# Performance work log

Hardware: AMD Instinct MI355X
Metric: run time of the kernel (lower is better)

## Reference

```python
import jax, jax.numpy as jnp
import numpy as np

N_NODES = 50000
N_EDGES = 640000
RAW = 128
HID = 256
COORD = 3


def setup_inputs() -> dict:
    key = jax.random.key(0)
    ks = jax.random.split(key, 20)

    def w(k, fan_in, fan_out):
        return (jax.random.normal(k, (fan_in, fan_out), jnp.float32)
                / np.float32(np.sqrt(fan_in)))

    return {
        "edge_index": jax.random.randint(ks[0], (2, N_EDGES), 0, N_NODES, jnp.int64)
        if jax.config.jax_enable_x64 else
        jax.random.randint(ks[0], (2, N_EDGES), 0, N_NODES, jnp.int32),
        "str_feature": jax.random.normal(ks[1], (N_NODES, RAW), jnp.float32),
        "coord_feature": jax.random.normal(ks[2], (N_NODES, COORD), jnp.float32),
        # msg_mlp: Linear(2*RAW+1 -> HID), SiLU, Linear(HID -> HID), SiLU
        "msg_w1": w(ks[3], 2 * RAW + 1, HID), "msg_b1": jnp.zeros((HID,), jnp.float32),
        "msg_w2": w(ks[4], HID, HID), "msg_b2": jnp.zeros((HID,), jnp.float32),
        # trans_mlp: Linear(HID->HID), SiLU, Linear(HID->HID), SiLU, Linear(HID->1, no bias, xavier gain=0.001)
        "tr_w1": w(ks[5], HID, HID), "tr_b1": jnp.zeros((HID,), jnp.float32),
        "tr_w2": w(ks[6], HID, HID), "tr_b2": jnp.zeros((HID,), jnp.float32),
        "tr_w3": w(ks[7], HID, 1) * np.float32(0.001),
        # posi_mlp: Linear(RAW+HID->HID), SiLU, Linear(HID->RAW)
        "posi_w1": w(ks[8], RAW + HID, HID), "posi_b1": jnp.zeros((HID,), jnp.float32),
        "posi_w2": w(ks[9], HID, RAW), "posi_b2": jnp.zeros((RAW,), jnp.float32),
    }


def reference(edge_index, str_feature, coord_feature,
              msg_w1, msg_b1, msg_w2, msg_b2,
              tr_w1, tr_b1, tr_w2, tr_b2, tr_w3,
              posi_w1, posi_b1, posi_w2, posi_b2):
    silu = jax.nn.silu
    row, col = edge_index[0], edge_index[1]
    n = str_feature.shape[0]

    # coord2dist
    coord_diff = coord_feature[row] - coord_feature[col]          # [E, 3]
    sqr_dist = jnp.sum(coord_diff * coord_diff, axis=1, keepdims=True)  # [E, 1]

    # msg_model
    edge_in = jnp.concatenate([str_feature[row], str_feature[col], sqr_dist], axis=1)
    msg = silu(silu(edge_in @ msg_w1 + msg_b1) @ msg_w2 + msg_b2)  # [E, HID]

    # coord_model: trans = coord_diff * trans_mlp(msg); x += segment_mean(trans, row)
    gate = silu(silu(msg @ tr_w1 + tr_b1) @ tr_w2 + tr_b2) @ tr_w3  # [E, 1]
    trans = coord_diff * gate                                       # [E, 3]
    trans_sum = jax.ops.segment_sum(trans, row, num_segments=n)     # [N, 3]
    cnt = jax.ops.segment_sum(jnp.ones((trans.shape[0],), trans.dtype), row,
                              num_segments=n)
    trans_mean = trans_sum / jnp.clip(cnt, 1.0)[:, None]
    coord_out = coord_feature + trans_mean

    # posi_model: p + posi_mlp([p, segment_sum(msg, row)])
    msg_sum = jax.ops.segment_sum(msg, row, num_segments=n)         # [N, HID]
    p_in = jnp.concatenate([str_feature, msg_sum], axis=1)
    str_out = str_feature + (silu(p_in @ posi_w1 + posi_b1) @ posi_w2 + posi_b2)

    return str_out, coord_out
```

## Files before the change

### kernel.cpp

```cpp
#include <hip/hip_runtime.h>

#define NN 50000
#define NE 640000

typedef __bf16 bf16x8 __attribute__((ext_vector_type(8)));
typedef short  short8 __attribute__((ext_vector_type(8)));
typedef float  f32x16 __attribute__((ext_vector_type(16)));
typedef float  f32x2  __attribute__((ext_vector_type(2)));
typedef float  f32x4  __attribute__((ext_vector_type(4)));

__device__ __forceinline__ short f2bf(float v) {
  unsigned u = __builtin_bit_cast(unsigned, v);
  u = (u + 0x7FFFu + ((u >> 16) & 1u)) >> 16;
  return (short)u;
}
__device__ __forceinline__ short f2bf_hw(float v) {
  return __builtin_bit_cast(short, (__bf16)v);
}
__device__ __forceinline__ float silu_f(float v) {
  float e = __builtin_amdgcn_exp2f(v * -1.44269504f);
  return v * __builtin_amdgcn_rcpf(1.0f + e);
}
__device__ __forceinline__ bf16x8 ld8(const short* p) {
  return *(const bf16x8*)(p);
}
__device__ __forceinline__ void atomic_add_f(float* p, float v) {
  __hip_atomic_fetch_add(p, v, __ATOMIC_RELAXED, __HIP_MEMORY_SCOPE_AGENT);
}

__global__ void egcl_prep(const float* __restrict__ mw1, const float* __restrict__ mb1,
                          const float* __restrict__ mw2, const float* __restrict__ mb2,
                          const float* __restrict__ tw1, const float* __restrict__ tb1,
                          const float* __restrict__ tw2, const float* __restrict__ tb2,
                          const float* __restrict__ pw1, const float* __restrict__ pw2,
                          const float* __restrict__ strf, const int* __restrict__ rowp,
                          short* __restrict__ w1t, short* __restrict__ w2t,
                          short* __restrict__ t1t, short* __restrict__ t2t,
                          short* __restrict__ p1t, short* __restrict__ p2t,
                          short* __restrict__ strb, int* __restrict__ deg)
{
  const int S0 = 71680, S2 = 98304, S3 = 32768, SS = NN * 128;
  const int total = 4 * S0 + S2 + S3 + SS + NE;
  int stride = gridDim.x * blockDim.x;
  for (int i = blockIdx.x * blockDim.x + threadIdx.x; i < total; i += stride) {
    int j = i;
    if (j < S0) { int n = j / 280, k = j - n * 280;
      float v = (k < 257) ? mw1[k * 256 + n] : ((k == 257) ? mb1[n] : 0.0f);
      w1t[j] = f2bf(v); continue; }
    j -= S0;
    if (j < S0) { int n = j / 280, k = j - n * 280;
      float v = (k < 256) ? mw2[k * 256 + n] : ((k == 257) ? mb2[n] : 0.0f);
      w2t[j] = f2bf(v); continue; }
    j -= S0;
    if (j < S0) { int n = j / 280, k = j - n * 280;
      float v = (k < 256) ? tw1[k * 256 + n] : ((k == 257) ? tb1[n] : 0.0f);
      t1t[j] = f2bf(v); continue; }
    j -= S0;
    if (j < S0) { int n = j / 280, k = j - n * 280;
      float v = (k < 256) ? tw2[k * 256 + n] : ((k == 257) ? tb2[n] : 0.0f);
      t2t[j] = f2bf(v); continue; }
    j -= S0;
    if (j < S2) { int n = j / 384, k = j - n * 384; p1t[j] = f2bf(pw1[k * 256 + n]); continue; }
    j -= S2;
    if (j < S3) { int n = j >> 8, k = j & 255; p2t[j] = f2bf(pw2[k * 128 + n]); continue; }
    j -= S3;
    if (j < SS) { strb[j] = f2bf(strf[j]); continue; }
    j -= SS;
    atomicAdd(deg + rowp[j], 1);
  }
}

__global__ __launch_bounds__(1024)
void egcl_scan(const int* __restrict__ deg, int* __restrict__ base)
{
  __shared__ int wsum[16], wincl[16];
  __shared__ int carry_s;
  const int tid = threadIdx.x, lane = tid & 63, w = tid >> 6;
  if (tid == 0) carry_s = 0;
  __syncthreads();
  for (int start = 0; start < NN; start += 1024) {
    const int i = start + tid;
    int v = (i < NN) ? deg[i] : 0;
    int s = v;
#pragma unroll
    for (int off = 1; off < 64; off <<= 1) {
      int t = __shfl_up(s, off);
      if (lane >= off) s += t;
    }
    if (lane == 63) wsum[w] = s;
    __syncthreads();
    if (w == 0) {
      int u = (lane < 16) ? wsum[lane] : 0;
#pragma unroll
      for (int off = 1; off < 16; off <<= 1) {
        int t = __shfl_up(u, off);
        if (lane >= off) u += t;
      }
      if (lane < 16) wincl[lane] = u;
    }
    __syncthreads();
    const int waveoff = wincl[w] - wsum[w];
    const int carry = carry_s;
    if (i < NN) base[i] = carry + waveoff + s - v;
    __syncthreads();
    if (tid == 0) carry_s = carry + wincl[15];
    __syncthreads();
  }
  if (tid == 0) base[NN] = NE;
}

__global__ void egcl_scatter(const int* __restrict__ rowp, const int* __restrict__ base,
                             int* __restrict__ cursor, int* __restrict__ eidg)
{
  int stride = gridDim.x * blockDim.x;
  for (int e = blockIdx.x * blockDim.x + threadIdx.x; e < NE; e += stride) {
    int r = rowp[e];
    int pos = base[r] + atomicAdd(cursor + r, 1);
    eidg[pos] = e;
  }
}


template<int NKS>
__device__ __forceinline__ void gemm64(const short* Ab, const short* __restrict__ WT,
                                       int wn, int lh, int l32, f32x16 acc[4])
{
  acc[0] = (f32x16)(0.0f); acc[1] = (f32x16)(0.0f);
  acc[2] = (f32x16)(0.0f); acc[3] = (f32x16)(0.0f);
  const short* arow = Ab + l32 * 280 + lh * 8;
  const short* brow = WT + (wn * 64 + l32) * 280 + lh * 8;
#pragma unroll
  for (int ks = 0; ks < NKS; ++ks) {
    const int kb = ks * 16;
    bf16x8 b0 = ld8(brow + kb);
    bf16x8 b1 = ld8(brow + 32 * 280 + kb);
    bf16x8 a0 = ld8(arow + kb);
    bf16x8 a1 = ld8(arow + 32 * 280 + kb);
    acc[0] = __builtin_amdgcn_mfma_f32_32x32x16_bf16(a0, b0, acc[0], 0, 0, 0);
    acc[1] = __builtin_amdgcn_mfma_f32_32x32x16_bf16(a1, b0, acc[1], 0, 0, 0);
    acc[2] = __builtin_amdgcn_mfma_f32_32x32x16_bf16(a0, b1, acc[2], 0, 0, 0);
    acc[3] = __builtin_amdgcn_mfma_f32_32x32x16_bf16(a1, b1, acc[3], 0, 0, 0);
  }
}

__device__ __forceinline__ void silu_acc(f32x16 acc[4], float b0, float b1)
{
#pragma unroll
  for (int i = 0; i < 4; ++i) {
    const float b = (i < 2) ? b0 : b1;
#pragma unroll
    for (int r = 0; r < 16; ++r) acc[i][r] = silu_f(acc[i][r] + b);
  }
}

__device__ __forceinline__ void write_acc(short* Ab, const f32x16 acc[4],
                                          int wn, int lh, int l32)
{
#pragma unroll
  for (int nh = 0; nh < 2; ++nh) {
    const int n = wn * 64 + nh * 32 + l32;
#pragma unroll
    for (int sm = 0; sm < 2; ++sm) {
      const f32x16& a = acc[nh * 2 + sm];
      short* dst = Ab + (sm * 32 + 4 * lh) * 280 + n;
#pragma unroll
      for (int j = 0; j < 8; ++j) {
        const int row = (j & 1) * 2 + 8 * (j >> 1);
        dst[row * 280]       = f2bf_hw(a[2 * j]);
        dst[(row + 1) * 280] = f2bf_hw(a[2 * j + 1]);
      }
    }
  }
}

__global__ __launch_bounds__(256, 4)
void egcl_edge(const int* __restrict__ eidx, const float* __restrict__ coord,
               const short* __restrict__ strb, const int* __restrict__ eidg,
               const int* __restrict__ base,
               const short* __restrict__ w1t, const short* __restrict__ w2t,
               const short* __restrict__ t1t, const short* __restrict__ t2t,
               const float* __restrict__ mb2v, const float* __restrict__ tb1v,
               const float* __restrict__ tb2v,
               const float* __restrict__ tr_w3,
               float* __restrict__ msg_sum, float* __restrict__ trans_sum)
{
  __shared__ short Ab[64 * 280];
  __shared__ int   rs_s[64], own_s[64];
  __shared__ float cdx_s[64], cdy_s[64], cdz_s[64], gate_s[64];

  const int tid  = threadIdx.x;
  const int lane = tid & 63, wave = tid >> 6;
  const int lh = lane >> 5, l32 = lane & 31;
  const int wn = wave;
  const int p0 = blockIdx.x * 64;
  const int* __restrict__ rowp = eidx;
  const int* __restrict__ colp = eidx + NE;

  const int nb = wn * 64 + l32;
  const float b2_0 = mb2v[nb], b2_1 = mb2v[nb + 32];
  const float b3_0 = tb1v[nb], b3_1 = tb1v[nb + 32];
  const float b4_0 = tb2v[nb], b4_1 = tb2v[nb + 32];

  if (tid < 64) {
    int e = eidg[p0 + tid];
    int r = rowp[e], c = colp[e];
    rs_s[tid] = r;
    const int wstart = p0 + (tid & ~31);
    own_s[tid] = (base[r] >= wstart) && (base[r + 1] <= wstart + 32) ? 1 : 0;
    float dx = coord[r * 3 + 0] - coord[c * 3 + 0];
    float dy = coord[r * 3 + 1] - coord[c * 3 + 1];
    float dz = coord[r * 3 + 2] - coord[c * 3 + 2];
    cdx_s[tid] = dx; cdy_s[tid] = dy; cdz_s[tid] = dz;
    short8 d8 = (short8)(short)0;
    d8[0] = f2bf(dx * dx + dy * dy + dz * dz);
    d8[1] = f2bf(1.0f);
    *(short8*)(Ab + tid * 280 + 256) = d8;
    *(short8*)(Ab + tid * 280 + 264) = (short8)(short)0;
    *(short8*)(Ab + tid * 280 + 272) = (short8)(short)0;
  }
#pragma unroll
  for (int it = 0; it < 8; ++it) {
    int i = tid + it * 256;
    int e = i >> 5, cc = i & 31;
    int eid = eidg[p0 + e];
    int node = (cc < 16) ? rowp[eid] : colp[eid];
    short8 v = *(const short8*)(strb + node * 128 + (cc & 15) * 8);
    *(short8*)(Ab + e * 280 + cc * 8) = v;
  }
  __syncthreads();

  f32x16 acc[4];

  gemm64<17>(Ab, w1t, wn, lh, l32, acc);
  silu_acc(acc, 0.0f, 0.0f);
  __syncthreads();
  write_acc(Ab, acc, wn, lh, l32);
  __syncthreads();

  gemm64<16>(Ab, w2t, wn, lh, l32, acc);
  silu_acc(acc, b2_0, b2_1);
  __syncthreads();
  write_acc(Ab, acc, wn, lh, l32);
  __syncthreads();

  gemm64<16>(Ab, t1t, wn, lh, l32, acc);
  silu_acc(acc, b3_0, b3_1);
  {
    const int cp  = tid & 127;
    const int e0w = (tid >> 7) * 32;
    float run0 = 0.0f, run1 = 0.0f;
    int prev = rs_s[e0w];
    int own  = own_s[e0w];
#pragma unroll 4
    for (int i = 0; i < 32; ++i) {
      const int idx = e0w + i;
      const int r = rs_s[idx];
      unsigned u = *(const unsigned*)(Ab + idx * 280 + cp * 2);
      float lo = __builtin_bit_cast(float, u << 16);
      float hi = __builtin_bit_cast(float, u & 0xFFFF0000u);
      if (r != prev) {
        if (own) {
          f32x2 v; v.x = run0; v.y = run1;
          *((f32x2*)msg_sum + prev * 128 + cp) = v;
        } else {
          atomic_add_f(msg_sum + prev * 256 + cp * 2 + 0, run0);
          atomic_add_f(msg_sum + prev * 256 + cp * 2 + 1, run1);
        }
        run0 = 0.0f; run1 = 0.0f; prev = r; own = own_s[idx];
      }
      run0 += lo; run1 += hi;
    }
    if (own) {
      f32x2 v; v.x = run0; v.y = run1;
      *((f32x2*)msg_sum + prev * 128 + cp) = v;
    } else {
      atomic_add_f(msg_sum + prev * 256 + cp * 2 + 0, run0);
      atomic_add_f(msg_sum + prev * 256 + cp * 2 + 1, run1);
    }
  }
  __syncthreads();
  write_acc(Ab, acc, wn, lh, l32);
  __syncthreads();

  gemm64<16>(Ab, t2t, wn, lh, l32, acc);
  silu_acc(acc, b4_0, b4_1);
  __syncthreads();
  write_acc(Ab, acc, wn, lh, l32);
  __syncthreads();

  {
    const int e = tid >> 2, p = tid & 3;
    const short* ap = Ab + e * 280 + p * 64;
    const float4* wp = (const float4*)(tr_w3 + p * 64);
    float s = 0.0f;
#pragma unroll
    for (int j = 0; j < 8; ++j) {
      bf16x8 av = ld8(ap + j * 8);
      float4 w0 = wp[2 * j], w1 = wp[2 * j + 1];
      s += (float)av[0] * w0.x + (float)av[1] * w0.y + (float)av[2] * w0.z + (float)av[3] * w0.w;
      s += (float)av[4] * w1.x + (float)av[5] * w1.y + (float)av[6] * w1.z + (float)av[7] * w1.w;
    }
    s += __shfl_xor(s, 1);
    s += __shfl_xor(s, 2);
    if (p == 0) gate_s[e] = s;
  }
  __syncthreads();
  if (tid < 64) {
    const int r = rs_s[tid];
    const float g = gate_s[tid];
    float vx = cdx_s[tid] * g, vy = cdy_s[tid] * g, vz = cdz_s[tid] * g;
#pragma unroll
    for (int off = 1; off < 64; off <<= 1) {
      int   rr = __shfl_up(r, off);
      float tx = __shfl_up(vx, off);
      float ty = __shfl_up(vy, off);
      float tz = __shfl_up(vz, off);
      if (tid >= off && rr == r) { vx += tx; vy += ty; vz += tz; }
    }
    int rn = __shfl_down(r, 1);
    if (tid == 63 || rn != r) {
      atomic_add_f(trans_sum + r * 3 + 0, vx);
      atomic_add_f(trans_sum + r * 3 + 1, vy);
      atomic_add_f(trans_sum + r * 3 + 2, vz);
    }
  }
}

__global__ __launch_bounds__(256, 3)
void egcl_node(const float* __restrict__ strf, const float* __restrict__ coord,
               const short* __restrict__ strb,
               const short* __restrict__ p1t, const short* __restrict__ p2t,
               const float* __restrict__ pb1, const float* __restrict__ pb2,
               const float* __restrict__ msg_sum, const float* __restrict__ trans_sum,
               const int* __restrict__ base, float* __restrict__ out)
{
  __shared__ short Ab[64 * 392];
  const int tid  = threadIdx.x;
  const int lane = tid & 63, wave = tid >> 6;
  const int quad = lane >> 4, l16 = lane & 15;
  const int n0 = blockIdx.x * 64;

#pragma unroll
  for (int it = 0; it < 4; ++it) {
    int i = tid + it * 256;
    int m = i >> 4, c = i & 15;
    int n = n0 + m;
    short8 v = (short8)(short)0;
    if (n < NN) v = *(const short8*)(strb + n * 128 + c * 8);
    *(short8*)(Ab + m * 392 + c * 8) = v;
  }
#pragma unroll
  for (int it = 0; it < 8; ++it) {
    int i = tid + it * 256;
    int m = i >> 5, c = i & 31;
    int n = n0 + m;
    short8 v = (short8)(short)0;
    if (n < NN) {
      const float* src = msg_sum + n * 256 + c * 8;
#pragma unroll
      for (int j = 0; j < 8; ++j) v[j] = f2bf_hw(src[j]);
    }
    *(short8*)(Ab + m * 392 + 128 + c * 8) = v;
  }
  __syncthreads();

  f32x4 acc[4][4];
#pragma unroll
  for (int nt = 0; nt < 4; ++nt)
#pragma unroll
    for (int mt = 0; mt < 4; ++mt) acc[nt][mt] = (f32x4)(0.0f);
#pragma unroll
  for (int ks = 0; ks < 12; ++ks) {
    const int kb = ks * 32 + quad * 8;
    bf16x8 b[4];
#pragma unroll
    for (int nt = 0; nt < 4; ++nt)
      b[nt] = ld8(p1t + (wave * 64 + nt * 16 + l16) * 384 + kb);
#pragma unroll
    for (int mt = 0; mt < 4; ++mt) {
      bf16x8 a = ld8(Ab + (mt * 16 + l16) * 392 + kb);
#pragma unroll
      for (int nt = 0; nt < 4; ++nt)
        acc[nt][mt] = __builtin_amdgcn_mfma_f32_16x16x32_bf16(a, b[nt], acc[nt][mt], 0, 0, 0);
    }
  }
  __syncthreads();
#pragma unroll
  for (int nt = 0; nt < 4; ++nt) {
    const int n = wave * 64 + nt * 16 + l16;
    const float bn = pb1[n];
#pragma unroll
    for (int mt = 0; mt < 4; ++mt)
#pragma unroll
      for (int r = 0; r < 4; ++r) {
        const int m = mt * 16 + quad * 4 + r;
        Ab[m * 392 + n] = f2bf_hw(silu_f(acc[nt][mt][r] + bn));
      }
  }
  __syncthreads();

  f32x4 a2[2][4];
#pragma unroll
  for (int nt = 0; nt < 2; ++nt)
#pragma unroll
    for (int mt = 0; mt < 4; ++mt) a2[nt][mt] = (f32x4)(0.0f);
#pragma unroll
  for (int ks = 0; ks < 8; ++ks) {
    const int kb = ks * 32 + quad * 8;
    bf16x8 b0 = ld8(p2t + (wave * 32 + l16) * 256 + kb);
    bf16x8 b1 = ld8(p2t + (wave * 32 + 16 + l16) * 256 + kb);
#pragma unroll
    for (int mt = 0; mt < 4; ++mt) {
      bf16x8 a = ld8(Ab + (mt * 16 + l16) * 392 + kb);
      a2[0][mt] = __builtin_amdgcn_mfma_f32_16x16x32_bf16(a, b0, a2[0][mt], 0, 0, 0);
      a2[1][mt] = __builtin_amdgcn_mfma_f32_16x16x32_bf16(a, b1, a2[1][mt], 0, 0, 0);
    }
  }
#pragma unroll
  for (int nt = 0; nt < 2; ++nt) {
    const int c = wave * 32 + nt * 16 + l16;
    const float bc = pb2[c];
#pragma unroll
    for (int mt = 0; mt < 4; ++mt)
#pragma unroll
      for (int r = 0; r < 4; ++r) {
        const int m = mt * 16 + quad * 4 + r;
        const int n = n0 + m;
        if (n < NN) out[n * 128 + c] = strf[n * 128 + c] + a2[nt][mt][r] + bc;
      }
  }
  if (tid < 64) {
    const int n = n0 + tid;
    if (n < NN) {
      float cv = (float)(base[n + 1] - base[n]); if (cv < 1.0f) cv = 1.0f;
      float inv = __builtin_amdgcn_rcpf(cv);
      out[NN * 128 + n * 3 + 0] = coord[n * 3 + 0] + trans_sum[n * 3 + 0] * inv;
      out[NN * 128 + n * 3 + 1] = coord[n * 3 + 1] + trans_sum[n * 3 + 1] * inv;
      out[NN * 128 + n * 3 + 2] = coord[n * 3 + 2] + trans_sum[n * 3 + 2] * inv;
    }
  }
}

extern "C" void kernel_launch(void* const* d_in, const int* in_sizes, int n_in,
                              void* d_out, int out_size, void* d_ws, size_t ws_size,
                              hipStream_t stream)
{
  const int*   eidx   = (const int*)d_in[0];
  const float* strf   = (const float*)d_in[1];
  const float* coord  = (const float*)d_in[2];
  const float* msg_w1 = (const float*)d_in[3];
  const float* msg_b1 = (const float*)d_in[4];
  const float* msg_w2 = (const float*)d_in[5];
  const float* msg_b2 = (const float*)d_in[6];
  const float* tr_w1  = (const float*)d_in[7];
  const float* tr_b1  = (const float*)d_in[8];
  const float* tr_w2  = (const float*)d_in[9];
  const float* tr_b2  = (const float*)d_in[10];
  const float* tr_w3  = (const float*)d_in[11];
  const float* posi_w1 = (const float*)d_in[12];
  const float* posi_b1 = (const float*)d_in[13];
  const float* posi_w2 = (const float*)d_in[14];
  const float* posi_b2 = (const float*)d_in[15];
  float* out = (float*)d_out;

  char* ws = (char*)d_ws;
  float* msg_sum   = (float*)ws;
  float* trans_sum = msg_sum + NN * 256;
  int*   deg       = (int*)(trans_sum + NN * 3);
  int*   cursor    = deg + NN;
  int*   base      = cursor + NN;
  int*   eidg      = base + NN + 8;
  short* strb = (short*)(eidg + NE);
  short* w1t  = strb + NN * 128;
  short* w2t  = w1t + 71680;
  short* t1t  = w2t + 71680;
  short* t2t  = t1t + 71680;
  short* p1t  = t2t + 71680;
  short* p2t  = p1t + 98304;

  const int* rowp = eidx;

  (void)hipMemsetAsync(ws, 0, (size_t)(NN * 256 + NN * 3 + NN + NN) * 4, stream);
  egcl_prep<<<2048, 256, 0, stream>>>(msg_w1, msg_b1, msg_w2, msg_b2,
                                      tr_w1, tr_b1, tr_w2, tr_b2,
                                      posi_w1, posi_w2,
                                      strf, rowp, w1t, w2t, t1t, t2t, p1t, p2t, strb, deg);
  egcl_scan<<<1, 1024, 0, stream>>>(deg, base);
  egcl_scatter<<<2560, 256, 0, stream>>>(rowp, base, cursor, eidg);
  egcl_edge<<<NE / 64, 256, 0, stream>>>(eidx, coord, strb, eidg, base,
                                         w1t, w2t, t1t, t2t,
                                         msg_b2, tr_b1, tr_b2, tr_w3,
                                         msg_sum, trans_sum);
  egcl_node<<<(NN + 63) / 64, 256, 0, stream>>>(strf, coord, strb, p1t, p2t,
                                                posi_b1, posi_b2,
                                                msg_sum, trans_sum, base, out);
}
```

Measured before the change: 1.040 ms.

## Keep edge MLP activations in registers per wave, computing transposed GEMMs

The edge kernel is restructured so each wave owns 32 edges and computes all 256 output features as W^T·X^T. Activations stay in registers as MFMA B-fragments, and lane-half swaps via shuffles replace the LDS round-trips and block-wide barriers between layers. Biases are folded into an extra K row, and the final gate dot-product is done in registers from a precomputed w3 table. The cost is much higher register pressure (launch bounds lowered to 2 blocks per CU) and every wave now streams the full weight matrices.

```diff
diff --git a/kernel.cpp b/kernel.cpp
--- a/kernel.cpp
+++ b/kernel.cpp
@@ -6,8 +6,7 @@
 typedef __bf16 bf16x8 __attribute__((ext_vector_type(8)));
 typedef short  short8 __attribute__((ext_vector_type(8)));
 typedef float  f32x16 __attribute__((ext_vector_type(16)));
-typedef float  f32x2  __attribute__((ext_vector_type(2)));
-typedef float  f32x4  __attribute__((ext_vector_type(4)));
+typedef unsigned u32x4 __attribute__((ext_vector_type(4)));
 
 __device__ __forceinline__ short f2bf(float v) {
   unsigned u = __builtin_bit_cast(unsigned, v);
@@ -17,6 +16,9 @@
 __device__ __forceinline__ short f2bf_hw(float v) {
   return __builtin_bit_cast(short, (__bf16)v);
 }
+__device__ __forceinline__ unsigned pack2(float a, float b) {
+  return (unsigned)(unsigned short)f2bf_hw(a) | ((unsigned)(unsigned short)f2bf_hw(b) << 16);
+}
 __device__ __forceinline__ float silu_f(float v) {
   float e = __builtin_amdgcn_exp2f(v * -1.44269504f);
   return v * __builtin_amdgcn_rcpf(1.0f + e);
@@ -32,15 +34,17 @@
                           const float* __restrict__ mw2, const float* __restrict__ mb2,
                           const float* __restrict__ tw1, const float* __restrict__ tb1,
                           const float* __restrict__ tw2, const float* __restrict__ tb2,
+                          const float* __restrict__ tw3,
                           const float* __restrict__ pw1, const float* __restrict__ pw2,
                           const float* __restrict__ strf, const int* __restrict__ rowp,
                           short* __restrict__ w1t, short* __restrict__ w2t,
                           short* __restrict__ t1t, short* __restrict__ t2t,
                           short* __restrict__ p1t, short* __restrict__ p2t,
+                          float* __restrict__ w3tab,
                           short* __restrict__ strb, int* __restrict__ deg)
 {
-  const int S0 = 71680, S2 = 98304, S3 = 32768, SS = NN * 128;
-  const int total = 4 * S0 + S2 + S3 + SS + NE;
+  const int S0 = 71680, S2 = 98304, S3 = 32768, S4 = 256, SS = NN * 128;
+  const int total = 4 * S0 + S2 + S3 + S4 + SS + NE;
   int stride = gridDim.x * blockDim.x;
   for (int i = blockIdx.x * blockDim.x + threadIdx.x; i < total; i += stride) {
     int j = i;
@@ -49,21 +53,25 @@
       w1t[j] = f2bf(v); continue; }
     j -= S0;
     if (j < S0) { int n = j / 280, k = j - n * 280;
-      float v = (k < 256) ? mw2[k * 256 + n] : ((k == 257) ? mb2[n] : 0.0f);
+      float v = (k < 256) ? mw2[k * 256 + n] : ((k == 256) ? mb2[n] : 0.0f);
       w2t[j] = f2bf(v); continue; }
     j -= S0;
     if (j < S0) { int n = j / 280, k = j - n * 280;
-      float v = (k < 256) ? tw1[k * 256 + n] : ((k == 257) ? tb1[n] : 0.0f);
+      float v = (k < 256) ? tw1[k * 256 + n] : ((k == 256) ? tb1[n] : 0.0f);
       t1t[j] = f2bf(v); continue; }
     j -= S0;
     if (j < S0) { int n = j / 280, k = j - n * 280;
-      float v = (k < 256) ? tw2[k * 256 + n] : ((k == 257) ? tb2[n] : 0.0f);
+      float v = (k < 256) ? tw2[k * 256 + n] : ((k == 256) ? tb2[n] : 0.0f);
       t2t[j] = f2bf(v); continue; }
     j -= S0;
     if (j < S2) { int n = j / 384, k = j - n * 384; p1t[j] = f2bf(pw1[k * 256 + n]); continue; }
     j -= S2;
     if (j < S3) { int n = j >> 8, k = j & 255; p2t[j] = f2bf(pw2[k * 128 + n]); continue; }
     j -= S3;
+    if (j < S4) { int lh = j >> 7, rem = j & 127, nt = rem >> 4, rr = rem & 15;
+      int n = nt * 32 + (rr & 3) + 8 * (rr >> 2) + 4 * lh;
+      w3tab[j] = tw3[n]; continue; }
+    j -= S4;
     if (j < SS) { strb[j] = f2bf(strf[j]); continue; }
     j -= SS;
     atomicAdd(deg + rowp[j], 1);
@@ -121,207 +129,188 @@
 }
 
 
-template<int NKS>
-__device__ __forceinline__ void gemm64(const short* Ab, const short* __restrict__ WT,
-                                       int wn, int lh, int l32, f32x16 acc[4])
-{
-  acc[0] = (f32x16)(0.0f); acc[1] = (f32x16)(0.0f);
-  acc[2] = (f32x16)(0.0f); acc[3] = (f32x16)(0.0f);
-  const short* arow = Ab + l32 * 280 + lh * 8;
-  const short* brow = WT + (wn * 64 + l32) * 280 + lh * 8;
-#pragma unroll
-  for (int ks = 0; ks < NKS; ++ks) {
-    const int kb = ks * 16;
-    bf16x8 b0 = ld8(brow + kb);
-    bf16x8 b1 = ld8(brow + 32 * 280 + kb);
-    bf16x8 a0 = ld8(arow + kb);
-    bf16x8 a1 = ld8(arow + 32 * 280 + kb);
-    acc[0] = __builtin_amdgcn_mfma_f32_32x32x16_bf16(a0, b0, acc[0], 0, 0, 0);
-    acc[1] = __builtin_amdgcn_mfma_f32_32x32x16_bf16(a1, b0, acc[1], 0, 0, 0);
-    acc[2] = __builtin_amdgcn_mfma_f32_32x32x16_bf16(a0, b1, acc[2], 0, 0, 0);
-    acc[3] = __builtin_amdgcn_mfma_f32_32x32x16_bf16(a1, b1, acc[3], 0, 0, 0);
-  }
-}
-
-__device__ __forceinline__ void silu_acc(f32x16 acc[4], float b0, float b1)
-{
-#pragma unroll
-  for (int i = 0; i < 4; ++i) {
-    const float b = (i < 2) ? b0 : b1;
-#pragma unroll
-    for (int r = 0; r < 16; ++r) acc[i][r] = silu_f(acc[i][r] + b);
-  }
-}
-
-__device__ __forceinline__ void write_acc(short* Ab, const f32x16 acc[4],
-                                          int wn, int lh, int l32)
-{
-#pragma unroll
-  for (int nh = 0; nh < 2; ++nh) {
-    const int n = wn * 64 + nh * 32 + l32;
-#pragma unroll
-    for (int sm = 0; sm < 2; ++sm) {
-      const f32x16& a = acc[nh * 2 + sm];
-      short* dst = Ab + (sm * 32 + 4 * lh) * 280 + n;
-#pragma unroll
-      for (int j = 0; j < 8; ++j) {
-        const int row = (j & 1) * 2 + 8 * (j >> 1);
-        dst[row * 280]       = f2bf_hw(a[2 * j]);
-        dst[(row + 1) * 280] = f2bf_hw(a[2 * j + 1]);
-      }
-    }
-  }
-}
-
-__global__ __launch_bounds__(256, 4)
+__device__ __forceinline__ bf16x8 frag4(unsigned a, unsigned b, unsigned c, unsigned d)
+{
+  u32x4 t; t[0] = a; t[1] = b; t[2] = c; t[3] = d;
+  return __builtin_bit_cast(bf16x8, t);
+}
+
+__device__ __forceinline__ void form_b(const f32x16 a[8], bf16x8 b[16], int lh)
+{
+#pragma unroll
+  for (int nt = 0; nt < 8; ++nt)
+#pragma unroll
+    for (int P = 0; P < 2; ++P) {
+      float s0 = silu_f(a[nt][8*P+0]), s1 = silu_f(a[nt][8*P+1]);
+      float s2 = silu_f(a[nt][8*P+2]), s3 = silu_f(a[nt][8*P+3]);
+      float s4 = silu_f(a[nt][8*P+4]), s5 = silu_f(a[nt][8*P+5]);
+      float s6 = silu_f(a[nt][8*P+6]), s7 = silu_f(a[nt][8*P+7]);
+      unsigned L0 = pack2(s0, s1), L1 = pack2(s2, s3);
+      unsigned H0 = pack2(s4, s5), H1 = pack2(s6, s7);
+      unsigned X0 = lh ? L0 : H0, X1 = lh ? L1 : H1;
+      unsigned Y0 = (unsigned)__shfl_xor((int)X0, 32);
+      unsigned Y1 = (unsigned)__shfl_xor((int)X1, 32);
+      unsigned W0 = lh ? Y0 : L0, W1 = lh ? Y1 : L1;
+      unsigned W2 = lh ? H0 : Y0, W3 = lh ? H1 : Y1;
+      b[2 * nt + P] = frag4(W0, W1, W2, W3);
+    }
+}
+
+__device__ __forceinline__ void gemmL(const short* __restrict__ WT,
+                                      const bf16x8 b[16], bf16x8 bks16,
+                                      int l32, int lh, f32x16 a[8])
+{
+#pragma unroll
+  for (int nt = 0; nt < 8; ++nt) a[nt] = (f32x16)(0.0f);
+  const short* wbase = WT + l32 * 280 + lh * 8;
+#pragma unroll
+  for (int ks = 0; ks < 17; ++ks) {
+    const bf16x8 bb = (ks < 16) ? b[ks] : bks16;
+#pragma unroll
+    for (int nt = 0; nt < 8; ++nt) {
+      bf16x8 w = ld8(wbase + nt * 32 * 280 + ks * 16);
+      a[nt] = __builtin_amdgcn_mfma_f32_32x32x16_bf16(w, bb, a[nt], 0, 0, 0);
+    }
+  }
+}
+
+__global__ __launch_bounds__(256, 2)
 void egcl_edge(const int* __restrict__ eidx, const float* __restrict__ coord,
                const short* __restrict__ strb, const int* __restrict__ eidg,
                const int* __restrict__ base,
                const short* __restrict__ w1t, const short* __restrict__ w2t,
                const short* __restrict__ t1t, const short* __restrict__ t2t,
-               const float* __restrict__ mb2v, const float* __restrict__ tb1v,
-               const float* __restrict__ tb2v,
-               const float* __restrict__ tr_w3,
+               const float* __restrict__ w3tab,
                float* __restrict__ msg_sum, float* __restrict__ trans_sum)
 {
-  __shared__ short Ab[64 * 280];
-  __shared__ int   rs_s[64], own_s[64];
-  __shared__ float cdx_s[64], cdy_s[64], cdz_s[64], gate_s[64];
+  __shared__ short msg_s[4][32 * 260];
+  __shared__ int   rs_w[4][32];
+  __shared__ int   own_w[4][32];
 
   const int tid  = threadIdx.x;
   const int lane = tid & 63, wave = tid >> 6;
   const int lh = lane >> 5, l32 = lane & 31;
-  const int wn = wave;
-  const int p0 = blockIdx.x * 64;
+  const int p0w = (blockIdx.x * 4 + wave) * 32;
   const int* __restrict__ rowp = eidx;
   const int* __restrict__ colp = eidx + NE;
 
-  const int nb = wn * 64 + l32;
-  const float b2_0 = mb2v[nb], b2_1 = mb2v[nb + 32];
-  const float b3_0 = tb1v[nb], b3_1 = tb1v[nb + 32];
-  const float b4_0 = tb2v[nb], b4_1 = tb2v[nb + 32];
-
-  if (tid < 64) {
-    int e = eidg[p0 + tid];
-    int r = rowp[e], c = colp[e];
-    rs_s[tid] = r;
-    const int wstart = p0 + (tid & ~31);
-    own_s[tid] = (base[r] >= wstart) && (base[r + 1] <= wstart + 32) ? 1 : 0;
-    float dx = coord[r * 3 + 0] - coord[c * 3 + 0];
-    float dy = coord[r * 3 + 1] - coord[c * 3 + 1];
-    float dz = coord[r * 3 + 2] - coord[c * 3 + 2];
-    cdx_s[tid] = dx; cdy_s[tid] = dy; cdz_s[tid] = dz;
-    short8 d8 = (short8)(short)0;
-    d8[0] = f2bf(dx * dx + dy * dy + dz * dz);
-    d8[1] = f2bf(1.0f);
-    *(short8*)(Ab + tid * 280 + 256) = d8;
-    *(short8*)(Ab + tid * 280 + 264) = (short8)(short)0;
-    *(short8*)(Ab + tid * 280 + 272) = (short8)(short)0;
-  }
-#pragma unroll
-  for (int it = 0; it < 8; ++it) {
-    int i = tid + it * 256;
-    int e = i >> 5, cc = i & 31;
-    int eid = eidg[p0 + e];
-    int node = (cc < 16) ? rowp[eid] : colp[eid];
-    short8 v = *(const short8*)(strb + node * 128 + (cc & 15) * 8);
-    *(short8*)(Ab + e * 280 + cc * 8) = v;
-  }
-  __syncthreads();
-
-  f32x16 acc[4];
-
-  gemm64<17>(Ab, w1t, wn, lh, l32, acc);
-  silu_acc(acc, 0.0f, 0.0f);
-  __syncthreads();
-  write_acc(Ab, acc, wn, lh, l32);
-  __syncthreads();
-
-  gemm64<16>(Ab, w2t, wn, lh, l32, acc);
-  silu_acc(acc, b2_0, b2_1);
-  __syncthreads();
-  write_acc(Ab, acc, wn, lh, l32);
-  __syncthreads();
-
-  gemm64<16>(Ab, t1t, wn, lh, l32, acc);
-  silu_acc(acc, b3_0, b3_1);
+  const int e = eidg[p0w + l32];
+  const int r = rowp[e], c = colp[e];
+  const float dx = coord[r * 3 + 0] - coord[c * 3 + 0];
+  const float dy = coord[r * 3 + 1] - coord[c * 3 + 1];
+  const float dz = coord[r * 3 + 2] - coord[c * 3 + 2];
+  const float dist = dx * dx + dy * dy + dz * dz;
+  if (lh == 0) {
+    rs_w[wave][l32]  = r;
+    own_w[wave][l32] = (base[r] >= p0w) && (base[r + 1] <= p0w + 32) ? 1 : 0;
+  }
+
+  bf16x8 b[16];
+#pragma unroll
+  for (int ks = 0; ks < 8; ++ks) b[ks]     = ld8(strb + r * 128 + ks * 16 + lh * 8);
+#pragma unroll
+  for (int ks = 0; ks < 8; ++ks) b[8 + ks] = ld8(strb + c * 128 + ks * 16 + lh * 8);
+  bf16x8 bL1;
   {
-    const int cp  = tid & 127;
-    const int e0w = (tid >> 7) * 32;
-    float run0 = 0.0f, run1 = 0.0f;
-    int prev = rs_s[e0w];
-    int own  = own_s[e0w];
-#pragma unroll 4
-    for (int i = 0; i < 32; ++i) {
-      const int idx = e0w + i;
-      const int r = rs_s[idx];
-      unsigned u = *(const unsigned*)(Ab + idx * 280 + cp * 2);
-      float lo = __builtin_bit_cast(float, u << 16);
-      float hi = __builtin_bit_cast(float, u & 0xFFFF0000u);
-      if (r != prev) {
-        if (own) {
-          f32x2 v; v.x = run0; v.y = run1;
-          *((f32x2*)msg_sum + prev * 128 + cp) = v;
-        } else {
-          atomic_add_f(msg_sum + prev * 256 + cp * 2 + 0, run0);
-          atomic_add_f(msg_sum + prev * 256 + cp * 2 + 1, run1);
-        }
-        run0 = 0.0f; run1 = 0.0f; prev = r; own = own_s[idx];
+    short8 s = (short8)(short)0;
+    if (lh == 0) { s[0] = f2bf(dist); s[1] = f2bf(1.0f); }
+    bL1 = __builtin_bit_cast(bf16x8, s);
+  }
+  bf16x8 bBias;
+  {
+    short8 s = (short8)(short)0;
+    if (lh == 0) s[0] = f2bf(1.0f);
+    bBias = __builtin_bit_cast(bf16x8, s);
+  }
+
+  f32x16 a[8];
+
+  gemmL(w1t, b, bL1, l32, lh, a);
+  form_b(a, b, lh);
+  gemmL(w2t, b, bBias, l32, lh, a);
+
+  {
+    short* mrow = &msg_s[wave][l32 * 260];
+#pragma unroll
+    for (int nt = 0; nt < 8; ++nt)
+#pragma unroll
+      for (int g = 0; g < 4; ++g) {
+        float v0 = silu_f(a[nt][4 * g + 0]), v1 = silu_f(a[nt][4 * g + 1]);
+        float v2 = silu_f(a[nt][4 * g + 2]), v3 = silu_f(a[nt][4 * g + 3]);
+        uint2 uu; uu.x = pack2(v0, v1); uu.y = pack2(v2, v3);
+        *(uint2*)(mrow + nt * 32 + g * 8 + lh * 4) = uu;
       }
-      run0 += lo; run1 += hi;
-    }
-    if (own) {
-      f32x2 v; v.x = run0; v.y = run1;
-      *((f32x2*)msg_sum + prev * 128 + cp) = v;
-    } else {
-      atomic_add_f(msg_sum + prev * 256 + cp * 2 + 0, run0);
-      atomic_add_f(msg_sum + prev * 256 + cp * 2 + 1, run1);
-    }
-  }
-  __syncthreads();
-  write_acc(Ab, acc, wn, lh, l32);
-  __syncthreads();
-
-  gemm64<16>(Ab, t2t, wn, lh, l32, acc);
-  silu_acc(acc, b4_0, b4_1);
-  __syncthreads();
-  write_acc(Ab, acc, wn, lh, l32);
-  __syncthreads();
-
-  {
-    const int e = tid >> 2, p = tid & 3;
-    const short* ap = Ab + e * 280 + p * 64;
-    const float4* wp = (const float4*)(tr_w3 + p * 64);
-    float s = 0.0f;
-#pragma unroll
-    for (int j = 0; j < 8; ++j) {
-      bf16x8 av = ld8(ap + j * 8);
-      float4 w0 = wp[2 * j], w1 = wp[2 * j + 1];
-      s += (float)av[0] * w0.x + (float)av[1] * w0.y + (float)av[2] * w0.z + (float)av[3] * w0.w;
-      s += (float)av[4] * w1.x + (float)av[5] * w1.y + (float)av[6] * w1.z + (float)av[7] * w1.w;
-    }
-    s += __shfl_xor(s, 1);
-    s += __shfl_xor(s, 2);
-    if (p == 0) gate_s[e] = s;
-  }
-  __syncthreads();
-  if (tid < 64) {
-    const int r = rs_s[tid];
-    const float g = gate_s[tid];
-    float vx = cdx_s[tid] * g, vy = cdy_s[tid] * g, vz = cdz_s[tid] * g;
-#pragma unroll
-    for (int off = 1; off < 64; off <<= 1) {
+  }
+  form_b(a, b, lh);
+  gemmL(t1t, b, bBias, l32, lh, a);
+  form_b(a, b, lh);
+  gemmL(t2t, b, bBias, l32, lh, a);
+
+  float g = 0.0f;
+#pragma unroll
+  for (int nt = 0; nt < 8; ++nt)
+#pragma unroll
+    for (int rg = 0; rg < 4; ++rg) {
+      const float4 w = *(const float4*)(w3tab + lh * 128 + nt * 16 + rg * 4);
+      g += silu_f(a[nt][4 * rg + 0]) * w.x + silu_f(a[nt][4 * rg + 1]) * w.y
+         + silu_f(a[nt][4 * rg + 2]) * w.z + silu_f(a[nt][4 * rg + 3]) * w.w;
+    }
+  g += __shfl_xor(g, 32);
+
+  if (lh == 0) {
+    float vx = dx * g, vy = dy * g, vz = dz * g;
+#pragma unroll
+    for (int off = 1; off < 32; off <<= 1) {
       int   rr = __shfl_up(r, off);
       float tx = __shfl_up(vx, off);
       float ty = __shfl_up(vy, off);
       float tz = __shfl_up(vz, off);
-      if (tid >= off && rr == r) { vx += tx; vy += ty; vz += tz; }
+      if (l32 >= off && rr == r) { vx += tx; vy += ty; vz += tz; }
     }
     int rn = __shfl_down(r, 1);
-    if (tid == 63 || rn != r) {
+    if (l32 == 31 || rn != r) {
       atomic_add_f(trans_sum + r * 3 + 0, vx);
       atomic_add_f(trans_sum + r * 3 + 1, vy);
       atomic_add_f(trans_sum + r * 3 + 2, vz);
+    }
+  }
+
+  {
+    const int c0 = lane * 4;
+    const short* mb = &msg_s[wave][0];
+    float r0 = 0.0f, r1 = 0.0f, r2 = 0.0f, r3 = 0.0f;
+    int prev = rs_w[wave][0];
+    int own  = own_w[wave][0];
+#pragma unroll 4
+    for (int i = 0; i < 32; ++i) {
+      const int ri = rs_w[wave][i];
+      uint2 u = *(const uint2*)(mb + i * 260 + c0);
+      float v0 = __builtin_bit_cast(float, u.x << 16);
+      float v1 = __builtin_bit_cast(float, u.x & 0xFFFF0000u);
+      float v2 = __builtin_bit_cast(float, u.y << 16);
+      float v3 = __builtin_bit_cast(float, u.y & 0xFFFF0000u);
+      if (ri != prev) {
+        if (own) {
+          float4 v; v.x = r0; v.y = r1; v.z = r2; v.w = r3;
+          *(float4*)(msg_sum + prev * 256 + c0) = v;
+        } else {
+          atomic_add_f(msg_sum + prev * 256 + c0 + 0, r0);
+          atomic_add_f(msg_sum + prev * 256 + c0 + 1, r1);
+          atomic_add_f(msg_sum + prev * 256 + c0 + 2, r2);
+          atomic_add_f(msg_sum + prev * 256 + c0 + 3, r3);
+        }
+        r0 = r1 = r2 = r3 = 0.0f; prev = ri; own = own_w[wave][i];
+      }
+      r0 += v0; r1 += v1; r2 += v2; r3 += v3;
+    }
+    if (own) {
+      float4 v; v.x = r0; v.y = r1; v.z = r2; v.w = r3;
+      *(float4*)(msg_sum + prev * 256 + c0) = v;
+    } else {
+      atomic_add_f(msg_sum + prev * 256 + c0 + 0, r0);
+      atomic_add_f(msg_sum + prev * 256 + c0 + 1, r1);
+      atomic_add_f(msg_sum + prev * 256 + c0 + 2, r2);
+      atomic_add_f(msg_sum + prev * 256 + c0 + 3, r3);
     }
   }
 }
@@ -340,6 +329,8 @@
   const int quad = lane >> 4, l16 = lane & 15;
   const int n0 = blockIdx.x * 64;
 
+  typedef float f32x4v __attribute__((ext_vector_type(4)));
+
 #pragma unroll
   for (int it = 0; it < 4; ++it) {
     int i = tid + it * 256;
@@ -364,24 +355,24 @@
   }
   __syncthreads();
 
-  f32x4 acc[4][4];
+  f32x4v acc[4][4];
 #pragma unroll
   for (int nt = 0; nt < 4; ++nt)
 #pragma unroll
-    for (int mt = 0; mt < 4; ++mt) acc[nt][mt] = (f32x4)(0.0f);
+    for (int mt = 0; mt < 4; ++mt) acc[nt][mt] = (f32x4v)(0.0f);
 #pragma unroll
   for (int ks = 0; ks < 12; ++ks) {
     const int kb = ks * 32 + quad * 8;
-    bf16x8 b[4];
+    bf16x8 bv[4];
 #pragma unroll
     for (int nt = 0; nt < 4; ++nt)
-      b[nt] = ld8(p1t + (wave * 64 + nt * 16 + l16) * 384 + kb);
+      bv[nt] = ld8(p1t + (wave * 64 + nt * 16 + l16) * 384 + kb);
 #pragma unroll
     for (int mt = 0; mt < 4; ++mt) {
-      bf16x8 a = ld8(Ab + (mt * 16 + l16) * 392 + kb);
+      bf16x8 av = ld8(Ab + (mt * 16 + l16) * 392 + kb);
 #pragma unroll
       for (int nt = 0; nt < 4; ++nt)
-        acc[nt][mt] = __builtin_amdgcn_mfma_f32_16x16x32_bf16(a, b[nt], acc[nt][mt], 0, 0, 0);
+        acc[nt][mt] = __builtin_amdgcn_mfma_f32_16x16x32_bf16(av, bv[nt], acc[nt][mt], 0, 0, 0);
     }
   }
   __syncthreads();
@@ -392,18 +383,18 @@
 #pragma unroll
     for (int mt = 0; mt < 4; ++mt)
 #pragma unroll
-      for (int r = 0; r < 4; ++r) {
-        const int m = mt * 16 + quad * 4 + r;
-        Ab[m * 392 + n] = f2bf_hw(silu_f(acc[nt][mt][r] + bn));
+      for (int rr = 0; rr < 4; ++rr) {
+        const int m = mt * 16 + quad * 4 + rr;
+        Ab[m * 392 + n] = f2bf_hw(silu_f(acc[nt][mt][rr] + bn));
       }
   }
   __syncthreads();
 
-  f32x4 a2[2][4];
+  f32x4v a2[2][4];
 #pragma unroll
   for (int nt = 0; nt < 2; ++nt)
 #pragma unroll
-    for (int mt = 0; mt < 4; ++mt) a2[nt][mt] = (f32x4)(0.0f);
+    for (int mt = 0; mt < 4; ++mt) a2[nt][mt] = (f32x4v)(0.0f);
 #pragma unroll
   for (int ks = 0; ks < 8; ++ks) {
     const int kb = ks * 32 + quad * 8;
@@ -411,22 +402,22 @@
     bf16x8 b1 = ld8(p2t + (wave * 32 + 16 + l16) * 256 + kb);
 #pragma unroll
     for (int mt = 0; mt < 4; ++mt) {
-      bf16x8 a = ld8(Ab + (mt * 16 + l16) * 392 + kb);
-      a2[0][mt] = __builtin_amdgcn_mfma_f32_16x16x32_bf16(a, b0, a2[0][mt], 0, 0, 0);
-      a2[1][mt] = __builtin_amdgcn_mfma_f32_16x16x32_bf16(a, b1, a2[1][mt], 0, 0, 0);
+      bf16x8 av = ld8(Ab + (mt * 16 + l16) * 392 + kb);
+      a2[0][mt] = __builtin_amdgcn_mfma_f32_16x16x32_bf16(av, b0, a2[0][mt], 0, 0, 0);
+      a2[1][mt] = __builtin_amdgcn_mfma_f32_16x16x32_bf16(av, b1, a2[1][mt], 0, 0, 0);
     }
   }
 #pragma unroll
   for (int nt = 0; nt < 2; ++nt) {
-    const int c = wave * 32 + nt * 16 + l16;
-    const float bc = pb2[c];
+    const int cc = wave * 32 + nt * 16 + l16;
+    const float bc = pb2[cc];
 #pragma unroll
     for (int mt = 0; mt < 4; ++mt)
 #pragma unroll
-      for (int r = 0; r < 4; ++r) {
-        const int m = mt * 16 + quad * 4 + r;
+      for (int rr = 0; rr < 4; ++rr) {
+        const int m = mt * 16 + quad * 4 + rr;
         const int n = n0 + m;
-        if (n < NN) out[n * 128 + c] = strf[n * 128 + c] + a2[nt][mt][r] + bc;
+        if (n < NN) out[n * 128 + cc] = strf[n * 128 + cc] + a2[nt][mt][rr] + bc;
       }
   }
   if (tid < 64) {
@@ -477,20 +468,21 @@
   short* t2t  = t1t + 71680;
   short* p1t  = t2t + 71680;
   short* p2t  = p1t + 98304;
+  float* w3tab = (float*)(((uintptr_t)(p2t + 32768) + 15) & ~(uintptr_t)15);
 
   const int* rowp = eidx;
 
   (void)hipMemsetAsync(ws, 0, (size_t)(NN * 256 + NN * 3 + NN + NN) * 4, stream);
   egcl_prep<<<2048, 256, 0, stream>>>(msg_w1, msg_b1, msg_w2, msg_b2,
-                                      tr_w1, tr_b1, tr_w2, tr_b2,
+                                      tr_w1, tr_b1, tr_w2, tr_b2, tr_w3,
                                       posi_w1, posi_w2,
-                                      strf, rowp, w1t, w2t, t1t, t2t, p1t, p2t, strb, deg);
+                                      strf, rowp, w1t, w2t, t1t, t2t, p1t, p2t,
+                                      w3tab, strb, deg);
   egcl_scan<<<1, 1024, 0, stream>>>(deg, base);
   egcl_scatter<<<2560, 256, 0, stream>>>(rowp, base, cursor, eidg);
-  egcl_edge<<<NE / 64, 256, 0, stream>>>(eidx, coord, strb, eidg, base,
-                                         w1t, w2t, t1t, t2t,
-                                         msg_b2, tr_b1, tr_b2, tr_w3,
-                                         msg_sum, trans_sum);
+  egcl_edge<<<NE / 128, 256, 0, stream>>>(eidx, coord, strb, eidg, base,
+                                          w1t, w2t, t1t, t2t, w3tab,
+                                          msg_sum, trans_sum);
   egcl_node<<<(NN + 63) / 64, 256, 0, stream>>>(strf, coord, strb, p1t, p2t,
                                                 posi_b1, posi_b2,
                                                 msg_sum, trans_sum, base, out);
```

New measurement: 2.035 ms. 95.7% more time.
